# Performance work log

Hardware: AMD Instinct MI355X
Metric: run time of the kernel (lower is better)

## Reference

```python
import jax, jax.numpy as jnp
import numpy as np

NUM_KEYS = 64

def setup_inputs() -> dict:
    key = jax.random.key(0)
    k1, k2 = jax.random.split(key)
    inputs = jax.random.randint(k1, (8, 4096, 1024), 0, NUM_KEYS, dtype=jnp.int32)
    # learned per-key bias (build() creates shape (num_keys,) for key_shape=[1])
    b = jax.random.normal(k2, (NUM_KEYS,), dtype=jnp.float32)
    # keys are sorted unique scalars (0..63), stored as float like the TF cast
    keys = jnp.arange(NUM_KEYS, dtype=jnp.float32)
    return {"inputs": inputs, "b": b, "keys": keys}


def reference(inputs, b, keys):
    # Original math: out = sum_k (inputs == keys[k]) * b[k], elementwise over inputs.
    # With unique sorted keys this is a gather: find the matching key index per
    # element and pick b there; elements matching no key contribute 0.
    # This avoids the O(num_keys * numel) broadcast blow-up of the TF graph.
    xf = inputs.astype(jnp.float32)
    K = keys.shape[0]
    idx = jnp.clip(jnp.searchsorted(keys, xf), 0, K - 1)  # [8,4096,1024]
    out = jnp.where(keys[idx] == xf, b[idx], jnp.float32(0.0))
    return out
```

## Files before the change

### kernel.cpp

```cpp
#include <hip/hip_runtime.h>

#define NKEYS 64

__global__ __launch_bounds__(256) void sel_xform_kernel(
    const int4* __restrict__ in,
    const float* __restrict__ b,
    const float* __restrict__ keys,
    float4* __restrict__ out,
    int nvec, int ntail, const int* __restrict__ in_tail, float* __restrict__ out_tail)
{
    __shared__ float t[NKEYS];
    const int tid = threadIdx.x;
    if (tid < NKEYS) t[tid] = 0.0f;
    __syncthreads();
    if (tid < NKEYS) {
        const float kv = keys[tid];
        const int iv = (int)kv;
        if ((float)iv == kv && iv >= 0 && iv < NKEYS) {
            t[iv] = b[tid];
        }
    }
    __syncthreads();

    int i = blockIdx.x * blockDim.x + tid;
    const int stride = gridDim.x * blockDim.x;
    for (; i < nvec; i += stride) {
        const int4 v = in[i];
        float4 o;
        o.x = ((unsigned)v.x < NKEYS) ? t[v.x] : 0.0f;
        o.y = ((unsigned)v.y < NKEYS) ? t[v.y] : 0.0f;
        o.z = ((unsigned)v.z < NKEYS) ? t[v.z] : 0.0f;
        o.w = ((unsigned)v.w < NKEYS) ? t[v.w] : 0.0f;
        out[i] = o;
    }

    if (blockIdx.x == 0 && tid < ntail) {
        const int v = in_tail[tid];
        out_tail[tid] = ((unsigned)v < NKEYS) ? t[v] : 0.0f;
    }
}

extern "C" void kernel_launch(void* const* d_in, const int* in_sizes, int n_in,
                              void* d_out, int out_size, void* d_ws, size_t ws_size,
                              hipStream_t stream) {
    const int*   x    = (const int*)d_in[0];
    const float* b    = (const float*)d_in[1];
    const float* keys = (const float*)d_in[2];
    float* out = (float*)d_out;

    const int n    = in_sizes[0];
    const int nvec = n >> 2;
    const int ntail = n & 3;

    const int block = 256;
    int grid = (nvec + block - 1) / block;
    if (grid < 1) grid = 1;

    sel_xform_kernel<<<grid, block, 0, stream>>>(
        (const int4*)x, b, keys, (float4*)out,
        nvec, ntail, x + (nvec << 2), out + (nvec << 2));
}
```

Before: 225.4 us.

## Use wave shuffles for table lookup, nontemporal stores, cap grid size

Each lane now holds one table entry in a register, and lookups go through cross-lane __shfl within the 64-wide wavefront instead of LDS gathers. Output is written with nontemporal stores to avoid polluting the cache. The grid is capped at 2048 blocks with a grid-stride loop, cutting the cost of launching blocks and rebuilding the table in each one. The kernel is memory bound, so the lookup change may matter little, and capping the grid could reduce memory parallelism.

```diff
diff --git a/kernel.cpp b/kernel.cpp
--- a/kernel.cpp
+++ b/kernel.cpp
@@ -22,16 +22,31 @@
     }
     __syncthreads();
 
-    int i = blockIdx.x * blockDim.x + tid;
+    const float tv = t[tid & 63];
+
     const int stride = gridDim.x * blockDim.x;
-    for (; i < nvec; i += stride) {
-        const int4 v = in[i];
-        float4 o;
-        o.x = ((unsigned)v.x < NKEYS) ? t[v.x] : 0.0f;
-        o.y = ((unsigned)v.y < NKEYS) ? t[v.y] : 0.0f;
-        o.z = ((unsigned)v.z < NKEYS) ? t[v.z] : 0.0f;
-        o.w = ((unsigned)v.w < NKEYS) ? t[v.w] : 0.0f;
-        out[i] = o;
+    for (int base = blockIdx.x * blockDim.x; base < nvec; base += stride) {
+        const int i = base + tid;
+        int4 v;
+        if (i < nvec) {
+            v = in[i];
+        } else {
+            v = make_int4(0, 0, 0, 0);
+        }
+        const float sx = __shfl(tv, v.x & 63);
+        const float sy = __shfl(tv, v.y & 63);
+        const float sz = __shfl(tv, v.z & 63);
+        const float sw = __shfl(tv, v.w & 63);
+        if (i < nvec) {
+            float4 o;
+            o.x = ((unsigned)v.x < NKEYS) ? sx : 0.0f;
+            o.y = ((unsigned)v.y < NKEYS) ? sy : 0.0f;
+            o.z = ((unsigned)v.z < NKEYS) ? sz : 0.0f;
+            o.w = ((unsigned)v.w < NKEYS) ? sw : 0.0f;
+            typedef float __attribute__((ext_vector_type(4))) f32x4;
+            __builtin_nontemporal_store(*reinterpret_cast<const f32x4*>(&o),
+                                        reinterpret_cast<f32x4*>(&out[i]));
+        }
     }
 
     if (blockIdx.x == 0 && tid < ntail) {
@@ -54,6 +69,7 @@
 
     const int block = 256;
     int grid = (nvec + block - 1) / block;
+    if (grid > 2048) grid = 2048;
     if (grid < 1) grid = 1;
 
     sel_xform_kernel<<<grid, block, 0, stream>>>(
```

New measurement: 232.7 us. 1.03x slower.
